# Performance work log

Measured on AMD Instinct MI355X. Metric: run time of the kernel, lower is better.

## Reference

```python
import jax, jax.numpy as jnp
import numpy as np

D = 128
N_COLS = 64
EPS = 1e-6
# op MLP index per feature token: mult, add, cos, absdiff, sub_ab, sub_ba, div_ab, div_ba
MLP_IDX = np.array([0, 1, 2, 3, 4, 4, 5, 5])


def setup_inputs() -> dict:
    key = jax.random.key(0)
    ks = jax.random.split(key, 16)
    B = 64
    pairs = np.array([(i, j) for i in range(N_COLS) for j in range(i + 1, N_COLS)], dtype=np.int32)
    P = pairs.shape[0]  # 2016
    s = 0.02
    inp = {
        "x": jax.random.normal(ks[0], (B, N_COLS, D), dtype=jnp.float32),
        "presence": jax.random.randint(ks[1], (B, N_COLS), 0, 2, dtype=jnp.int32),
        "idx_i": jnp.asarray(pairs[:, 0]),
        "idx_j": jnp.asarray(pairs[:, 1]),
        # 6 op MLPs (multiply, add, cosine, abs_diff, subtract, divide): d -> d/2 -> d
        "ops_W1": jax.random.normal(ks[2], (6, D, D // 2), dtype=jnp.float32) * s,
        "ops_b1": jnp.zeros((6, D // 2), dtype=jnp.float32),
        "ops_W2": jax.random.normal(ks[3], (6, D // 2, D), dtype=jnp.float32) * s,
        "ops_b2": jnp.zeros((6, D), dtype=jnp.float32),
        # presence MLP: 4 -> d/2 -> d
        "pres_W1": jax.random.normal(ks[4], (4, D // 2), dtype=jnp.float32) * s,
        "pres_b1": jnp.zeros((D // 2,), dtype=jnp.float32),
        "pres_W2": jax.random.normal(ks[5], (D // 2, D), dtype=jnp.float32) * s,
        "pres_b2": jnp.zeros((D,), dtype=jnp.float32),
        # fusion MLP: 9d -> 2d -> d
        "fus_W1": jax.random.normal(ks[6], (9 * D, 2 * D), dtype=jnp.float32) * s,
        "fus_b1": jnp.zeros((2 * D,), dtype=jnp.float32),
        "fus_W2": jax.random.normal(ks[7], (2 * D, D), dtype=jnp.float32) * s,
        "fus_b2": jnp.zeros((D,), dtype=jnp.float32),
    }
    return inp


def reference(x, presence, idx_i, idx_j,
              ops_W1, ops_b1, ops_W2, ops_b2,
              pres_W1, pres_b1, pres_W2, pres_b2,
              fus_W1, fus_b1, fus_W2, fus_b2):
    B = x.shape[0]
    P = idx_i.shape[0]
    A = x[:, idx_i]  # [B, P, D]
    Bv = x[:, idx_j]  # [B, P, D]
    An = A / (jnp.linalg.norm(A, axis=-1, keepdims=True) + EPS)
    Bn = Bv / (jnp.linalg.norm(Bv, axis=-1, keepdims=True) + EPS)
    # 8 elementwise relation features [8, B, P, D]
    feats = jnp.stack([
        A * Bv,                 # multiply
        A + Bv,                 # add
        An * Bn,                # cosine (elementwise normalized product)
        jnp.abs(A - Bv),        # abs diff
        A - Bv,                 # subtract A->B
        Bv - A,                 # subtract B->A
        A / (Bv + EPS),         # divide A/B
        Bv / (A + EPS),         # divide B/A
    ])
    W1 = ops_W1[MLP_IDX]  # [8, D, D/2]
    b1 = ops_b1[MLP_IDX]
    W2 = ops_W2[MLP_IDX]
    b2 = ops_b2[MLP_IDX]
    h = jax.nn.relu(jnp.einsum('kbpd,kdh->kbph', feats, W1) + b1[:, None, None, :])
    tok = jnp.einsum('kbph,khd->kbpd', h, W2) + b2[:, None, None, :]  # [8, B, P, D]
    # presence flags [B, P, 4]
    pa = presence[:, idx_i].astype(x.dtype)
    pb = presence[:, idx_j].astype(x.dtype)
    flags = jnp.stack([pa * pb, pa * (1 - pb), (1 - pa) * pb, (1 - pa) * (1 - pb)], axis=-1)
    ptok = jax.nn.relu(flags @ pres_W1 + pres_b1) @ pres_W2 + pres_b2  # [B, P, D]
    # concat 9 tokens -> fusion MLP -> 1 token per pair
    cat = jnp.concatenate([jnp.transpose(tok, (1, 2, 0, 3)).reshape(B, P, 8 * D), ptok], axis=-1)
    out = jax.nn.relu(cat @ fus_W1 + fus_b1) @ fus_W2 + fus_b2  # [B, P, D]
    return out
```

## Files before the change

kernel.cpp:

```cpp
#include <hip/hip_runtime.h>

#define EPS 1e-6f

using bfrag = __attribute__((ext_vector_type(8))) short;
using hfrag = __attribute__((ext_vector_type(8))) _Float16;
using ffrag = __attribute__((ext_vector_type(4))) float;
typedef unsigned short ushortT;

#define MFMA(a, b, c) __builtin_amdgcn_mfma_f32_16x16x32_bf16((a), (b), (c), 0, 0, 0)
#define MFMA16(a, b, c) __builtin_amdgcn_mfma_f32_16x16x32_f16((a), (b), (c), 0, 0, 0)

__device__ __forceinline__ ushortT bf_hi(float x) {
  unsigned u = __builtin_bit_cast(unsigned, x);
  return (ushortT)((u + 0x7FFFu + ((u >> 16) & 1u)) >> 16);
}
__device__ __forceinline__ float uaf(unsigned u) { return __builtin_bit_cast(float, u); }
__device__ __forceinline__ unsigned cvtpk(float a, float b) {
  unsigned d;
  asm("v_cvt_pk_bf16_f32 %0, %1, %2" : "=v"(d) : "v"(a), "v"(b));
  return d;
}
__device__ __forceinline__ unsigned pkf16(float a, float b) {
  unsigned d;
  asm("v_cvt_pkrtz_f16_f32 %0, %1, %2" : "=v"(d) : "v"(a), "v"(b));
  return d;
}
__device__ __forceinline__ int op_of(int k) { return (k < 4) ? k : ((k >> 1) + 2); }

__global__ void prologue(const float* __restrict__ ops_W1,
                         const float* __restrict__ ops_W2,
                         const float* __restrict__ ops_b2,
                         const float* __restrict__ pres_W1,
                         const float* __restrict__ pres_b1,
                         const float* __restrict__ pres_W2,
                         const float* __restrict__ pres_b2,
                         const float* __restrict__ fus_W1,
                         const float* __restrict__ fus_b1,
                         const float* __restrict__ fus_W2,
                         ushortT* __restrict__ Gp,
                         ushortT* __restrict__ W1p,
                         ushortT* __restrict__ W2p,
                         float* __restrict__ cb) {
  const int blk = blockIdx.x;
  const int tid = threadIdx.x;

  if (blk < 512) {
    int r = blk, n = tid;
    int slot = r >> 6;
    const int KMAP[8] = {0, 2, 3, 4, 1, 5, 6, 7};
    int k = KMAP[slot];
    int op = op_of(k);
    const float* w2 = ops_W2 + (size_t)(op * 64 + (r & 63)) * 128;
    const float* w1 = fus_W1 + (size_t)(k * 128) * 256 + n;
    float a0 = 0.f, a1 = 0.f, a2 = 0.f, a3 = 0.f;
#pragma unroll 8
    for (int d = 0; d < 128; d += 4) {
      a0 = fmaf(w2[d], w1[(size_t)d * 256], a0);
      a1 = fmaf(w2[d + 1], w1[(size_t)(d + 1) * 256], a1);
      a2 = fmaf(w2[d + 2], w1[(size_t)(d + 2) * 256], a2);
      a3 = fmaf(w2[d + 3], w1[(size_t)(d + 3) * 256], a3);
    }
    float acc = (a0 + a1) + (a2 + a3);
    ushortT outv;
    if (slot < 6) {
      _Float16 hv = (_Float16)acc;
      outv = __builtin_bit_cast(ushortT, hv);
    } else {
      outv = bf_hi(acc);
    }
    int nt = n >> 4, kk = r >> 5, quad = (r >> 3) & 3, j = r & 7;
    int lane = quad * 16 + (n & 15);
    Gp[((nt * 16 + kk) * 64 + lane) * 8 + j] = outv;
  } else if (blk < 544) {
    int gid = (blk - 512) * 256 + tid;
    int lane = gid & 63, kk = (gid >> 6) & 3, nt = (gid >> 8) & 3, k = gid >> 10;
    int op = op_of(k);
    int col = nt * 16 + (lane & 15);
#pragma unroll
    for (int j = 0; j < 8; ++j) {
      int d = kk * 32 + ((lane >> 4) & 3) * 8 + j;
      float w = ops_W1[((size_t)op * 128 + d) * 64 + col];
      ushortT outv;
      if (k < 6) {
        _Float16 hv = (_Float16)w;
        outv = __builtin_bit_cast(ushortT, hv);
      } else {
        outv = bf_hi(w);
      }
      W1p[gid * 8 + j] = outv;
    }
  } else if (blk < 560) {
    int gid = (blk - 544) * 256 + tid;
    int lane = gid & 63, kk = (gid >> 6) & 7, nt = gid >> 9;
    int col = nt * 16 + (lane & 15);
#pragma unroll
    for (int j = 0; j < 8; ++j) {
      int d = kk * 32 + ((lane >> 4) & 3) * 8 + j;
      W2p[gid * 8 + j] = bf_hi(fus_W2[(size_t)d * 128 + col]);
    }
  } else {
    int c = blk - 560, n = tid;
    __shared__ float hrelu[64];
    __shared__ float ptok[128];
    if (n < 64) hrelu[n] = fmaxf(pres_W1[c * 64 + n] + pres_b1[n], 0.f);
    __syncthreads();
    if (n < 128) {
      float p0 = pres_b2[n], p1 = 0.f;
#pragma unroll 8
      for (int hh = 0; hh < 64; hh += 2) {
        p0 = fmaf(hrelu[hh], pres_W2[hh * 128 + n], p0);
        p1 = fmaf(hrelu[hh + 1], pres_W2[(hh + 1) * 128 + n], p1);
      }
      ptok[n] = p0 + p1;
    }
    __syncthreads();
    float acc = fus_b1[n];
#pragma unroll 4
    for (int d = 0; d < 128; ++d)
      acc = fmaf(ptok[d], fus_W1[(size_t)(1024 + d) * 256 + n], acc);
    float acc2 = 0.f;
    for (int k = 0; k < 8; ++k) {
      int op = op_of(k);
#pragma unroll 4
      for (int d = 0; d < 128; ++d)
        acc2 = fmaf(ops_b2[op * 128 + d], fus_W1[(size_t)(k * 128 + d) * 256 + n], acc2);
    }
    cb[c * 256 + n] = acc + acc2;
  }
}

__device__ __forceinline__ void ldX(const float* Xrow, int quad, float (&r)[32]) {
#pragma unroll
  for (int kk = 0; kk < 4; ++kk) {
    float4 t0 = *(const float4*)(Xrow + kk * 32 + quad * 8);
    float4 t1 = *(const float4*)(Xrow + kk * 32 + quad * 8 + 4);
    r[kk * 8 + 0] = t0.x; r[kk * 8 + 1] = t0.y; r[kk * 8 + 2] = t0.z; r[kk * 8 + 3] = t0.w;
    r[kk * 8 + 4] = t1.x; r[kk * 8 + 5] = t1.y; r[kk * 8 + 6] = t1.z; r[kk * 8 + 7] = t1.w;
  }
}

struct Frag2 {
  bfrag h[4];
  bfrag l[4];
};

union U4 {
  unsigned u[4];
  bfrag b;
};

#define FM_MUL 0
#define FM_ADD 1
#define FM_SUB 2
#define FM_ABS 3
#define FM_DAB 4
#define FM_DBA 5

template <int M>
__device__ __forceinline__ void buildFragsF16(const float (&af)[32], const float (&bf)[32],
                                              bfrag (&h)[4]) {
#pragma unroll
  for (int kk = 0; kk < 4; ++kk) {
    U4 uh;
#pragma unroll
    for (int p = 0; p < 4; ++p) {
      float a0 = af[kk * 8 + 2 * p],     b0 = bf[kk * 8 + 2 * p];
      float a1 = af[kk * 8 + 2 * p + 1], b1 = bf[kk * 8 + 2 * p + 1];
      float f0, f1;
      if constexpr (M == FM_MUL)      { f0 = a0 * b0; f1 = a1 * b1; }
      else if constexpr (M == FM_ADD) { f0 = a0 + b0; f1 = a1 + b1; }
      else if constexpr (M == FM_SUB) { f0 = a0 - b0; f1 = a1 - b1; }
      else                            { f0 = fabsf(a0 - b0); f1 = fabsf(a1 - b1); }
      uh.u[p] = pkf16(f0, f1);
    }
    h[kk] = uh.b;
  }
}

template <int M>
__device__ __forceinline__ void buildFrags(const float (&af)[32], const float (&bf)[32],
                                           Frag2& fr) {
#pragma unroll
  for (int kk = 0; kk < 4; ++kk) {
    U4 uh, ul;
#pragma unroll
    for (int p = 0; p < 4; ++p) {
      float a0 = af[kk * 8 + 2 * p],     b0 = bf[kk * 8 + 2 * p];
      float a1 = af[kk * 8 + 2 * p + 1], b1 = bf[kk * 8 + 2 * p + 1];
      float f0, f1;
      if constexpr (M == FM_DAB) {
        f0 = a0 * __builtin_amdgcn_rcpf(b0 + EPS);
        f1 = a1 * __builtin_amdgcn_rcpf(b1 + EPS);
      } else {
        f0 = b0 * __builtin_amdgcn_rcpf(a0 + EPS);
        f1 = b1 * __builtin_amdgcn_rcpf(a1 + EPS);
      }
      unsigned dh = cvtpk(f0, f1);
      float r0 = f0 - uaf(dh << 16);
      float r1 = f1 - uaf(dh & 0xFFFF0000u);
      uh.u[p] = dh;
      ul.u[p] = cvtpk(r0, r1);
    }
    fr.h[kk] = uh.b;
    fr.l[kk] = ul.b;
  }
}

template <int K>
__device__ __forceinline__ void mmAllF16(const bfrag (&h)[4], int lane,
                                         const ushortT* __restrict__ W1p, ffrag (&s)[4]) {
  const ushortT* wp = W1p + (K * 16) * 512 + lane * 8;
  bfrag wa[4], wb[4];
#pragma unroll
  for (int kk = 0; kk < 4; ++kk) wa[kk] = *(const bfrag*)(wp + kk * 512);
#pragma unroll
  for (int nt = 0; nt < 4; ++nt) {
    if (nt < 3) {
      bfrag (&wn)[4] = (nt & 1) ? wa : wb;
#pragma unroll
      for (int kk = 0; kk < 4; ++kk)
        wn[kk] = *(const bfrag*)(wp + (nt + 1) * 2048 + kk * 512);
    }
    const bfrag (&wc)[4] = (nt & 1) ? wb : wa;
    ffrag acc = {0.f, 0.f, 0.f, 0.f};
#pragma unroll
    for (int kk = 0; kk < 4; ++kk)
      acc = MFMA16(__builtin_bit_cast(hfrag, h[kk]), __builtin_bit_cast(hfrag, wc[kk]), acc);
    s[nt] = acc;
  }
}

template <int K>
__device__ __forceinline__ void mmAll(const Frag2& fr, int lane,
                                      const ushortT* __restrict__ W1p, ffrag (&s)[4]) {
  const ushortT* wp = W1p + (K * 16) * 512 + lane * 8;
  bfrag wa[4], wb[4];
#pragma unroll
  for (int kk = 0; kk < 4; ++kk) wa[kk] = *(const bfrag*)(wp + kk * 512);
#pragma unroll
  for (int nt = 0; nt < 4; ++nt) {
    if (nt < 3) {
      bfrag (&wn)[4] = (nt & 1) ? wa : wb;
#pragma unroll
      for (int kk = 0; kk < 4; ++kk)
        wn[kk] = *(const bfrag*)(wp + (nt + 1) * 2048 + kk * 512);
    }
    const bfrag (&wc)[4] = (nt & 1) ? wb : wa;
    ffrag acc = {0.f, 0.f, 0.f, 0.f};
#pragma unroll
    for (int kk = 0; kk < 4; ++kk) {
      acc = MFMA(fr.h[kk], wc[kk], acc);
      acc = MFMA(fr.l[kk], wc[kk], acc);
    }
    s[nt] = acc;
  }
}

__device__ __forceinline__ void ldBias(const float* __restrict__ ops_b1, int OP, int c0,
                                       float (&bb)[4]) {
#pragma unroll
  for (int nt = 0; nt < 4; ++nt) bb[nt] = ops_b1[OP * 64 + nt * 16 + c0];
}

__device__ __forceinline__ void storeHf(ffrag s, float scl, float bias, int rbase, int col,
                                        ushortT (*Hh)[136]) {
  float v[4];
#pragma unroll
  for (int i = 0; i < 4; ++i) v[i] = fmaxf(fmaf(s[i], scl, bias), 0.f);
#pragma unroll
  for (int p = 0; p < 2; ++p) {
    unsigned d = pkf16(v[2 * p], v[2 * p + 1]);
    Hh[rbase + 2 * p][col] = (ushortT)(d & 0xFFFFu);
    Hh[rbase + 2 * p + 1][col] = (ushortT)(d >> 16);
  }
}

__device__ __forceinline__ void storeHf4(const ffrag (&s)[4], float scl, const float (&bb)[4],
                                         int rbase, int colbase, int c0,
                                         ushortT (*Hh)[136]) {
#pragma unroll
  for (int nt = 0; nt < 4; ++nt)
    storeHf(s[nt], scl, bb[nt], rbase, colbase + nt * 16 + c0, Hh);
}

__device__ __forceinline__ void storeH(ffrag s, float bias, int rbase, int col,
                                       ushortT (*Hh)[136], ushortT (*Hl)[136]) {
  float v[4];
#pragma unroll
  for (int i = 0; i < 4; ++i) v[i] = fmaxf(s[i] + bias, 0.f);
#pragma unroll
  for (int p = 0; p < 2; ++p) {
    unsigned dh = cvtpk(v[2 * p], v[2 * p + 1]);
    float r0 = v[2 * p] - uaf(dh << 16);
    float r1 = v[2 * p + 1] - uaf(dh & 0xFFFF0000u);
    unsigned dl = cvtpk(r0, r1);
    Hh[rbase + 2 * p][col] = (ushortT)(dh & 0xFFFFu);
    Hh[rbase + 2 * p + 1][col] = (ushortT)(dh >> 16);
    Hl[rbase + 2 * p][col] = (ushortT)(dl & 0xFFFFu);
    Hl[rbase + 2 * p + 1][col] = (ushortT)(dl >> 16);
  }
}

__device__ __forceinline__ void storeH4(const ffrag (&s)[4], const float (&bb)[4],
                                        int rbase, int colbase, int c0,
                                        ushortT (*Hh)[136], ushortT (*Hl)[136]) {
#pragma unroll
  for (int nt = 0; nt < 4; ++nt)
    storeH(s[nt], bb[nt], rbase, colbase + nt * 16 + c0, Hh, Hl);
}

__device__ __forceinline__ void p3roundF16(int r, int wv, int lane, int quad, int c0,
                                           ushortT (*Hh)[136],
                                           const ushortT* __restrict__ Gp,
                                           ffrag (&u)[4], ffrag (&v)[4]) {
  bfrag g[4][4];
  const ushortT* gp = Gp + ((wv * 64 + r * 4) * 64 + lane) * 8;
#pragma unroll
  for (int nt4 = 0; nt4 < 4; ++nt4)
#pragma unroll
    for (int kk = 0; kk < 4; ++kk)
      g[nt4][kk] = *(const bfrag*)(gp + nt4 * 8192 + kk * 512);
#pragma unroll
  for (int kk = 0; kk < 4; ++kk) {
    hfrag ah0 = __builtin_bit_cast(hfrag, *(const bfrag*)&Hh[c0][kk * 32 + quad * 8]);
    hfrag ah1 = __builtin_bit_cast(hfrag, *(const bfrag*)&Hh[16 + c0][kk * 32 + quad * 8]);
#pragma unroll
    for (int nt4 = 0; nt4 < 4; ++nt4) {
      u[nt4] = MFMA16(ah0, __builtin_bit_cast(hfrag, g[nt4][kk]), u[nt4]);
      v[nt4] = MFMA16(ah1, __builtin_bit_cast(hfrag, g[nt4][kk]), v[nt4]);
    }
  }
}

__device__ __forceinline__ void p3round(int r, int wv, int lane, int quad, int c0,
                                        ushortT (*Hh)[136], ushortT (*Hl)[136],
                                        const ushortT* __restrict__ Gp,
                                        ffrag (&u)[4], ffrag (&v)[4]) {
  bfrag g[4][4];
  const ushortT* gp = Gp + ((wv * 64 + r * 4) * 64 + lane) * 8;
#pragma unroll
  for (int nt4 = 0; nt4 < 4; ++nt4)
#pragma unroll
    for (int kk = 0; kk < 4; ++kk)
      g[nt4][kk] = *(const bfrag*)(gp + nt4 * 8192 + kk * 512);
#pragma unroll
  for (int kk = 0; kk < 4; ++kk) {
    bfrag ah0 = *(const bfrag*)&Hh[c0][kk * 32 + quad * 8];
    bfrag al0 = *(const bfrag*)&Hl[c0][kk * 32 + quad * 8];
    bfrag ah1 = *(const bfrag*)&Hh[16 + c0][kk * 32 + quad * 8];
    bfrag al1 = *(const bfrag*)&Hl[16 + c0][kk * 32 + quad * 8];
#pragma unroll
    for (int nt4 = 0; nt4 < 4; ++nt4) {
      u[nt4] = MFMA(ah0, g[nt4][kk], u[nt4]);
      u[nt4] = MFMA(al0, g[nt4][kk], u[nt4]);
      v[nt4] = MFMA(ah1, g[nt4][kk], v[nt4]);
      v[nt4] = MFMA(al1, g[nt4][kk], v[nt4]);
    }
  }
}

__global__ __launch_bounds__(256, 3)
void drel_main(const float* __restrict__ x, const int* __restrict__ presence,
               const int* __restrict__ idx_i, const int* __restrict__ idx_j,
               const float* __restrict__ ops_b1, const float* __restrict__ fus_b2,
               const ushortT* __restrict__ W1p, const ushortT* __restrict__ Gp,
               const ushortT* __restrict__ W2p, const float* __restrict__ cbias,
               float* __restrict__ out) {
  __shared__ __align__(16) char smem[51328];
  float   (*Xs)[132]  = reinterpret_cast<float(*)[132]>(smem);
  ushortT (*Hh)[136]  = reinterpret_cast<ushortT(*)[136]>(smem + 33792);
  ushortT (*Hl)[136]  = reinterpret_cast<ushortT(*)[136]>(smem + 42496);
  ushortT (*Dh)[264]  = reinterpret_cast<ushortT(*)[264]>(smem + 33792);
  int* sCombo = reinterpret_cast<int*>(smem + 51200);

  const int tid = threadIdx.x;
  const int wv = tid >> 6, lane = tid & 63, quad = lane >> 4, c0 = lane & 15;
  const int wtile = wv & 1;
  const int wrole = wv >> 1;

  const int blk = blockIdx.x;
  const int b = blk / 63;
  const int p0 = (blk % 63) * 32;

  const float* xb = x + (size_t)b * 64 * 128;
#pragma unroll
  for (int it = 0; it < 8; ++it) {
    int i = tid + it * 256;
    int row = i >> 5, c4 = (i & 31) * 4;
    *(float4*)&Xs[row][c4] = *(const float4*)(xb + row * 128 + c4);
  }
  if (tid < 32) {
    int p = p0 + tid;
    int pa = presence[b * 64 + idx_i[p]];
    int pb = presence[b * 64 + idx_j[p]];
    sCombo[tid] = pa ? (pb ? 0 : 1) : (pb ? 2 : 3);
  }

  const int rI = idx_i[p0 + wtile * 16 + c0];
  const int rJ = idx_j[p0 + wtile * 16 + c0];
  const int rbase = wtile * 16 + quad * 4;

  ffrag u[4], v[4];
  __syncthreads();
  {
    int comb0[4], comb1[4];
#pragma unroll
    for (int i = 0; i < 4; ++i) {
      comb0[i] = sCombo[quad * 4 + i];
      comb1[i] = sCombo[16 + quad * 4 + i];
    }
#pragma unroll
    for (int nt4 = 0; nt4 < 4; ++nt4) {
      int col = (wv * 4 + nt4) * 16 + c0;
#pragma unroll
      for (int i = 0; i < 4; ++i) {
        u[nt4][i] = cbias[comb0[i] * 256 + col];
        v[nt4][i] = cbias[comb1[i] * 256 + col];
      }
    }
  }

  float af[32], bf[32];
  bfrag fh[4];
  ffrag s4[4];

  {
    ldX(Xs[rI], quad, af); ldX(Xs[rJ], quad, bf);
    buildFragsF16<FM_MUL>(af, bf, fh);
    ffrag s[4];
    float bb[4];
    if (wrole == 0) {
      ldBias(ops_b1, 0, c0, bb);
      mmAllF16<0>(fh, lane, W1p, s);
      storeHf4(s, 1.f, bb, rbase, 0, c0, Hh);
    } else {
      float sa = 0.f, sb = 0.f;
#pragma unroll
      for (int q = 0; q < 32; ++q) { sa = fmaf(af[q], af[q], sa); sb = fmaf(bf[q], bf[q], sb); }
      sa += __shfl_xor(sa, 16); sb += __shfl_xor(sb, 16);
      sa += __shfl_xor(sa, 32); sb += __shfl_xor(sb, 32);
      float scl = (1.f / (sqrtf(sa) + EPS)) * (1.f / (sqrtf(sb) + EPS));
      ldBias(ops_b1, 2, c0, bb);
      mmAllF16<2>(fh, lane, W1p, s);
      storeHf4(s, scl, bb, rbase, 64, c0, Hh);
    }
  }
  __syncthreads();
  p3roundF16(0, wv, lane, quad, c0, Hh, Gp, u, v);
  __syncthreads();

  {
    ldX(Xs[rI], quad, af); ldX(Xs[rJ], quad, bf);
    float bb[4];
    if (wrole == 0) {
      buildFragsF16<FM_ABS>(af, bf, fh);
      ffrag s[4];
      ldBias(ops_b1, 3, c0, bb);
      mmAllF16<3>(fh, lane, W1p, s);
      storeHf4(s, 1.f, bb, rbase, 0, c0, Hh);
    } else {
      buildFragsF16<FM_SUB>(af, bf, fh);
      ldBias(ops_b1, 4, c0, bb);
      mmAllF16<4>(fh, lane, W1p, s4);
      storeHf4(s4, 1.f, bb, rbase, 64, c0, Hh);
    }
  }
  __syncthreads();
  p3roundF16(1, wv, lane, quad, c0, Hh, Gp, u, v);
  __syncthreads();

  {
    float bb[4];
    if (wrole == 0) {
      ldX(Xs[rI], quad, af); ldX(Xs[rJ], quad, bf);
      buildFragsF16<FM_ADD>(af, bf, fh);
      ffrag s[4];
      ldBias(ops_b1, 1, c0, bb);
      mmAllF16<1>(fh, lane, W1p, s);
      storeHf4(s, 1.f, bb, rbase, 0, c0, Hh);
    } else {
      ldBias(ops_b1, 4, c0, bb);
      storeHf4(s4, -1.f, bb, rbase, 64, c0, Hh);
    }
  }
  __syncthreads();
  p3roundF16(2, wv, lane, quad, c0, Hh, Gp, u, v);
  __syncthreads();

  {
    ldX(Xs[rI], quad, af); ldX(Xs[rJ], quad, bf);
    Frag2 fr;
    ffrag s[4];
    float bb[4];
    ldBias(ops_b1, 5, c0, bb);
    if (wrole == 0) {
      buildFrags<FM_DAB>(af, bf, fr);
      mmAll<6>(fr, lane, W1p, s);
      storeH4(s, bb, rbase, 0, c0, Hh, Hl);
    } else {
      buildFrags<FM_DBA>(af, bf, fr);
      mmAll<7>(fr, lane, W1p, s);
      storeH4(s, bb, rbase, 64, c0, Hh, Hl);
    }
  }
  __syncthreads();
  p3round(3, wv, lane, quad, c0, Hh, Hl, Gp, u, v);
  __syncthreads();

#pragma unroll
  for (int nt4 = 0; nt4 < 4; ++nt4) {
    int col = (wv * 4 + nt4) * 16 + c0;
#pragma unroll
    for (int p = 0; p < 2; ++p) {
      unsigned du = cvtpk(fmaxf(u[nt4][2 * p], 0.f), fmaxf(u[nt4][2 * p + 1], 0.f));
      Dh[quad * 4 + 2 * p][col] = (ushortT)(du & 0xFFFFu);
      Dh[quad * 4 + 2 * p + 1][col] = (ushortT)(du >> 16);
      unsigned dv = cvtpk(fmaxf(v[nt4][2 * p], 0.f), fmaxf(v[nt4][2 * p + 1], 0.f));
      Dh[16 + quad * 4 + 2 * p][col] = (ushortT)(dv & 0xFFFFu);
      Dh[16 + quad * 4 + 2 * p + 1][col] = (ushortT)(dv >> 16);
    }
  }
  __syncthreads();

  ffrag o[2], q[2];
#pragma unroll
  for (int nt2 = 0; nt2 < 2; ++nt2) {
    float bias = fus_b2[(wv * 2 + nt2) * 16 + c0];
    o[nt2] = ffrag{bias, bias, bias, bias};
    q[nt2] = o[nt2];
  }
#pragma unroll
  for (int kk = 0; kk < 8; ++kk) {
    bfrag dh0 = *(const bfrag*)&Dh[c0][kk * 32 + quad * 8];
    bfrag dh1 = *(const bfrag*)&Dh[16 + c0][kk * 32 + quad * 8];
#pragma unroll
    for (int nt2 = 0; nt2 < 2; ++nt2) {
      bfrag w = *(const bfrag*)(W2p + (((wv * 2 + nt2) * 8 + kk) * 64 + lane) * 8);
      o[nt2] = MFMA(dh0, w, o[nt2]);
      q[nt2] = MFMA(dh1, w, q[nt2]);
    }
  }
#pragma unroll
  for (int nt2 = 0; nt2 < 2; ++nt2) {
    int col = (wv * 2 + nt2) * 16 + c0;
#pragma unroll
    for (int i = 0; i < 4; ++i) {
      int row = quad * 4 + i;
      out[(size_t)(b * 2016 + p0 + row) * 128 + col] = o[nt2][i];
      out[(size_t)(b * 2016 + p0 + 16 + row) * 128 + col] = q[nt2][i];
    }
  }
}

extern "C" void kernel_launch(void* const* d_in, const int* in_sizes, int n_in,
                              void* d_out, int out_size, void* d_ws, size_t ws_size,
                              hipStream_t stream) {
  const float* x        = (const float*)d_in[0];
  const int*   presence = (const int*)d_in[1];
  const int*   idx_i    = (const int*)d_in[2];
  const int*   idx_j    = (const int*)d_in[3];
  const float* ops_W1   = (const float*)d_in[4];
  const float* ops_b1   = (const float*)d_in[5];
  const float* ops_W2   = (const float*)d_in[6];
  const float* ops_b2   = (const float*)d_in[7];
  const float* pres_W1  = (const float*)d_in[8];
  const float* pres_b1  = (const float*)d_in[9];
  const float* pres_W2  = (const float*)d_in[10];
  const float* pres_b2  = (const float*)d_in[11];
  const float* fus_W1   = (const float*)d_in[12];
  const float* fus_b1   = (const float*)d_in[13];
  const float* fus_W2   = (const float*)d_in[14];
  const float* fus_b2   = (const float*)d_in[15];

  char* ws = (char*)d_ws;
  ushortT* Gp  = (ushortT*)(ws);
  ushortT* W1p = (ushortT*)(ws + 262144);
  ushortT* W2p = (ushortT*)(ws + 393216);
  float*   CB  = (float*)(ws + 458752);

  prologue<<<564, 256, 0, stream>>>(ops_W1, ops_W2, ops_b2, pres_W1, pres_b1,
                                    pres_W2, pres_b2, fus_W1, fus_b1, fus_W2,
                                    Gp, W1p, W2p, CB);
  drel_main<<<4032, 256, 0, stream>>>(x, presence, idx_i, idx_j, ops_b1, fus_b2,
                                      W1p, Gp, W2p, CB, (float*)d_out);
}
```

Measured before the change: 241.2 us.

## Stage only referenced x rows in LDS and raise occupancy to 4 blocks

Each block now builds a bitmask of the rows its 32 pairs reference. It compacts those rows into slots and loads only them into shared memory, sized for at most 40 rows instead of all 64. This shrinks LDS per block from about 51KB to 39KB and cuts redundant global loads, and launch bounds are raised to 4 blocks per CU to use the freed space. The cost is extra barriers and LDS atomics during setup, plus a tighter register budget that could cause spills.

```diff
diff --git a/kernel.cpp b/kernel.cpp
--- a/kernel.cpp
+++ b/kernel.cpp
@@ -129,6 +129,8 @@
   }
 }
 
+#define XS_ROWS 40
+
 __device__ __forceinline__ void ldX(const float* Xrow, int quad, float (&r)[32]) {
 #pragma unroll
   for (int kk = 0; kk < 4; ++kk) {
@@ -359,19 +361,22 @@
   }
 }
 
-__global__ __launch_bounds__(256, 3)
+__global__ __launch_bounds__(256, 4)
 void drel_main(const float* __restrict__ x, const int* __restrict__ presence,
                const int* __restrict__ idx_i, const int* __restrict__ idx_j,
                const float* __restrict__ ops_b1, const float* __restrict__ fus_b2,
                const ushortT* __restrict__ W1p, const ushortT* __restrict__ Gp,
                const ushortT* __restrict__ W2p, const float* __restrict__ cbias,
                float* __restrict__ out) {
-  __shared__ __align__(16) char smem[51328];
+  __shared__ __align__(16) char smem[39168];
   float   (*Xs)[132]  = reinterpret_cast<float(*)[132]>(smem);
-  ushortT (*Hh)[136]  = reinterpret_cast<ushortT(*)[136]>(smem + 33792);
-  ushortT (*Hl)[136]  = reinterpret_cast<ushortT(*)[136]>(smem + 42496);
-  ushortT (*Dh)[264]  = reinterpret_cast<ushortT(*)[264]>(smem + 33792);
-  int* sCombo = reinterpret_cast<int*>(smem + 51200);
+  ushortT (*Hh)[136]  = reinterpret_cast<ushortT(*)[136]>(smem + 21120);
+  ushortT (*Hl)[136]  = reinterpret_cast<ushortT(*)[136]>(smem + 29824);
+  ushortT (*Dh)[264]  = reinterpret_cast<ushortT(*)[264]>(smem + 21120);
+  int* sCombo = reinterpret_cast<int*>(smem + 38528);
+  unsigned* maskW = reinterpret_cast<unsigned*>(smem + 38656);
+  int* rowLocal = reinterpret_cast<int*>(smem + 38664);
+  int* rowOf = reinterpret_cast<int*>(smem + 38920);
 
   const int tid = threadIdx.x;
   const int wv = tid >> 6, lane = tid & 63, quad = lane >> 4, c0 = lane & 15;
@@ -382,26 +387,39 @@
   const int b = blk / 63;
   const int p0 = (blk % 63) * 32;
 
-  const float* xb = x + (size_t)b * 64 * 128;
-#pragma unroll
-  for (int it = 0; it < 8; ++it) {
-    int i = tid + it * 256;
-    int row = i >> 5, c4 = (i & 31) * 4;
-    *(float4*)&Xs[row][c4] = *(const float4*)(xb + row * 128 + c4);
-  }
+  if (tid < 2) maskW[tid] = 0;
+  __syncthreads();
   if (tid < 32) {
     int p = p0 + tid;
-    int pa = presence[b * 64 + idx_i[p]];
-    int pb = presence[b * 64 + idx_j[p]];
+    int ri = idx_i[p], rj = idx_j[p];
+    int pa = presence[b * 64 + ri];
+    int pb = presence[b * 64 + rj];
     sCombo[tid] = pa ? (pb ? 0 : 1) : (pb ? 2 : 3);
-  }
-
-  const int rI = idx_i[p0 + wtile * 16 + c0];
-  const int rJ = idx_j[p0 + wtile * 16 + c0];
+    atomicOr(&maskW[ri >> 5], 1u << (ri & 31));
+    atomicOr(&maskW[rj >> 5], 1u << (rj & 31));
+  }
+  __syncthreads();
+  const unsigned long long mask =
+      ((unsigned long long)maskW[1] << 32) | (unsigned long long)maskW[0];
+  const int nrows = __popcll(mask);
+  if (tid < 64 && ((mask >> tid) & 1)) {
+    int slot = __popcll(mask & ((1ull << tid) - 1ull));
+    rowLocal[tid] = slot;
+    rowOf[slot] = tid;
+  }
+  __syncthreads();
+
+  const float* xb = x + (size_t)b * 64 * 128;
+  for (int s = tid; s < nrows * 32; s += 256) {
+    int row = s >> 5, c4 = (s & 31) * 4;
+    *(float4*)&Xs[row][c4] = *(const float4*)(xb + (size_t)rowOf[row] * 128 + c4);
+  }
+
+  const int rI = rowLocal[idx_i[p0 + wtile * 16 + c0]];
+  const int rJ = rowLocal[idx_j[p0 + wtile * 16 + c0]];
   const int rbase = wtile * 16 + quad * 4;
 
   ffrag u[4], v[4];
-  __syncthreads();
   {
     int comb0[4], comb1[4];
 #pragma unroll
@@ -419,6 +437,7 @@
       }
     }
   }
+  __syncthreads();
 
   float af[32], bf[32];
   bfrag fh[4];
```

Measured after the change: 271.3 us. +12.5%, slower.
